# Kernel optimization log

Hardware: AMD Instinct MI355X
Metric: run time of the kernel (lower is better)

Reference implementation:

```python
import jax, jax.numpy as jnp
import numpy as np

EPS = 1e-6


def setup_inputs() -> dict:
    key = jax.random.key(0)
    k1, k2, k3 = jax.random.split(key, 3)
    B, L, H, D = 4, 4096, 16, 64
    return {
        "queries": jax.random.normal(k1, (B, L, H, D), dtype=jnp.float32),
        "keys": jax.random.normal(k2, (B, L, H, D), dtype=jnp.float32),
        "values": jax.random.normal(k3, (B, L, H, D), dtype=jnp.float32),
        "attn_mask": jnp.zeros((1,), dtype=bool),  # unused, matches torch signature
    }


def reference(queries, keys, values, attn_mask):
    # [B, L, H, D] -> [B, H, L, D]
    q = jax.nn.sigmoid(jnp.transpose(queries, (0, 2, 1, 3)))
    k = jax.nn.sigmoid(jnp.transpose(keys, (0, 2, 1, 3)))
    v = jnp.transpose(values, (0, 2, 1, 3))
    L = q.shape[2]
    S = k.shape[2]

    # flow normalizers (incoming / outgoing)
    normalizer_row = 1.0 / jnp.einsum('nhld,nhd->nhl', q + EPS, k.sum(axis=2) + EPS)
    normalizer_col = 1.0 / jnp.einsum('nhsd,nhd->nhs', k + EPS, q.sum(axis=2) + EPS)

    # competitive refinement
    row_refine = jnp.einsum(
        'nhld,nhd->nhl', q + EPS, (k * normalizer_col[..., None]).sum(axis=2) + EPS)
    col_refine = jnp.einsum(
        'nhsd,nhd->nhs', k + EPS, (q * normalizer_row[..., None]).sum(axis=2) + EPS)
    row_refine = jax.nn.sigmoid(row_refine * (float(L) / float(S)))
    col_refine = jax.nn.softmax(col_refine, axis=-1) * S

    # kv: [B, H, D, D]
    kv = jnp.einsum('nhsd,nhse->nhde', k, v * col_refine[..., None])
    x = jnp.einsum('nhld,nhde->nhle', q, kv)
    x = x * normalizer_row[..., None] * row_refine[..., None]
    # back to [B, L, H, D]
    return jnp.transpose(x, (0, 2, 1, 3))
```

## Files before the change

kernel.cpp:

```cpp
#include <hip/hip_runtime.h>
#include <math.h>
#include <stdint.h>

#define B_ 4
#define L_ 4096
#define H_ 16
#define EPSF 1e-6f
#define STR 66
#define STRO 68

typedef short bf16x8 __attribute__((ext_vector_type(8)));
typedef float f32x4 __attribute__((ext_vector_type(4)));
union FragU { uint32_t u[4]; bf16x8 v; };

__device__ __forceinline__ float sigf(float x) { return 1.0f / (1.0f + __expf(-x)); }

__device__ __forceinline__ uint32_t packhl(float x) {
    uint32_t xb = __float_as_uint(x);
    uint32_t hb = xb & 0xFFFF0000u;
    float lo = x - __uint_as_float(hb);
    return (hb >> 16) | (__float_as_uint(lo) & 0xFFFF0000u);
}

__device__ __forceinline__ void buildfrag(const uint32_t w[8], bf16x8& hi, bf16x8& lo) {
    FragU H, L;
#pragma unroll
    for (int t = 0; t < 4; ++t) {
        H.u[t] = __builtin_amdgcn_perm(w[2 * t + 1], w[2 * t], 0x05040100u);
        L.u[t] = __builtin_amdgcn_perm(w[2 * t + 1], w[2 * t], 0x07060302u);
    }
    hi = H.v; lo = L.v;
}

#define MFMA3(acc, ahi, alo, bhi, blo)                                        \
    acc = __builtin_amdgcn_mfma_f32_16x16x32_bf16(ahi, bhi, acc, 0, 0, 0);    \
    acc = __builtin_amdgcn_mfma_f32_16x16x32_bf16(ahi, blo, acc, 0, 0, 0);    \
    acc = __builtin_amdgcn_mfma_f32_16x16x32_bf16(alo, bhi, acc, 0, 0, 0);

__global__ __launch_bounds__(256, 8) void k_ksum(const float* __restrict__ K,
                                                 float* __restrict__ ksum) {
    int bh = blockIdx.x, b = bh >> 4, h = bh & 15;
    int t = threadIdx.x, lane = t & 63, w = t >> 6;
    int q4 = lane >> 4, i16 = lane & 15;
    int r0 = blockIdx.y * 128 + w * 32;
    float a0 = 0.f, a1 = 0.f, a2 = 0.f, a3 = 0.f;
#pragma unroll
    for (int ib = 0; ib < 2; ++ib) {
        float4 x[4];
#pragma unroll
        for (int j = 0; j < 4; ++j) {
            int r = r0 + (ib * 4 + j) * 4 + q4;
            x[j] = *(const float4*)(K + (((size_t)b * L_ + r) * H_ + h) * 64 + 4 * i16);
        }
#pragma unroll
        for (int j = 0; j < 4; ++j) {
            a0 += sigf(x[j].x); a1 += sigf(x[j].y);
            a2 += sigf(x[j].z); a3 += sigf(x[j].w);
        }
    }
#pragma unroll
    for (int m = 16; m < 64; m <<= 1) {
        a0 += __shfl_xor(a0, m, 64); a1 += __shfl_xor(a1, m, 64);
        a2 += __shfl_xor(a2, m, 64); a3 += __shfl_xor(a3, m, 64);
    }
    if (q4 == 0) {
        atomicAdd(&ksum[bh * 64 + 4 * i16 + 0], a0);
        atomicAdd(&ksum[bh * 64 + 4 * i16 + 1], a1);
        atomicAdd(&ksum[bh * 64 + 4 * i16 + 2], a2);
        atomicAdd(&ksum[bh * 64 + 4 * i16 + 3], a3);
    }
}

__global__ __launch_bounds__(256, 6) void k_qpass(const float* __restrict__ Q,
                                                  const float* __restrict__ ksum,
                                                  float* __restrict__ qsum,
                                                  float* __restrict__ qn) {
    int bh = blockIdx.x, b = bh >> 4, h = bh & 15;
    int t = threadIdx.x, lane = t & 63, w = t >> 6;
    int q4 = lane >> 4, i16 = lane & 15;
    int r0 = blockIdx.y * 128 + w * 32;
    float4 ks4 = *(const float4*)(ksum + bh * 64 + 4 * i16);
    ks4.x += EPSF; ks4.y += EPSF; ks4.z += EPSF; ks4.w += EPSF;
    float qs0 = 0.f, qs1 = 0.f, qs2 = 0.f, qs3 = 0.f;
    float qa0 = 0.f, qa1 = 0.f, qa2 = 0.f, qa3 = 0.f;
#pragma unroll
    for (int ib = 0; ib < 2; ++ib) {
        float4 x[4];
#pragma unroll
        for (int j = 0; j < 4; ++j) {
            int r = r0 + (ib * 4 + j) * 4 + q4;
            x[j] = *(const float4*)(Q + (((size_t)b * L_ + r) * H_ + h) * 64 + 4 * i16);
        }
#pragma unroll
        for (int j = 0; j < 4; ++j) {
            float s0 = sigf(x[j].x), s1 = sigf(x[j].y), s2 = sigf(x[j].z), s3 = sigf(x[j].w);
            float pa = (s0 + EPSF) * ks4.x + (s1 + EPSF) * ks4.y +
                       (s2 + EPSF) * ks4.z + (s3 + EPSF) * ks4.w;
#pragma unroll
            for (int m = 1; m < 16; m <<= 1) pa += __shfl_xor(pa, m, 64);
            float nr = __builtin_amdgcn_rcpf(pa);
            qs0 += s0; qs1 += s1; qs2 += s2; qs3 += s3;
            qa0 += s0 * nr; qa1 += s1 * nr; qa2 += s2 * nr; qa3 += s3 * nr;
        }
    }
#pragma unroll
    for (int m = 16; m < 64; m <<= 1) {
        qs0 += __shfl_xor(qs0, m, 64); qs1 += __shfl_xor(qs1, m, 64);
        qs2 += __shfl_xor(qs2, m, 64); qs3 += __shfl_xor(qs3, m, 64);
        qa0 += __shfl_xor(qa0, m, 64); qa1 += __shfl_xor(qa1, m, 64);
        qa2 += __shfl_xor(qa2, m, 64); qa3 += __shfl_xor(qa3, m, 64);
    }
    if (q4 == 0) {
        atomicAdd(&qsum[bh * 64 + 4 * i16 + 0], qs0);
        atomicAdd(&qsum[bh * 64 + 4 * i16 + 1], qs1);
        atomicAdd(&qsum[bh * 64 + 4 * i16 + 2], qs2);
        atomicAdd(&qsum[bh * 64 + 4 * i16 + 3], qs3);
        atomicAdd(&qn[bh * 64 + 4 * i16 + 0], qa0);
        atomicAdd(&qn[bh * 64 + 4 * i16 + 1], qa1);
        atomicAdd(&qn[bh * 64 + 4 * i16 + 2], qa2);
        atomicAdd(&qn[bh * 64 + 4 * i16 + 3], qa3);
    }
}

__global__ __launch_bounds__(256, 4) void k_kv(const float* __restrict__ K,
                                               const float* __restrict__ V,
                                               const float* __restrict__ qsum,
                                               const float* __restrict__ qn,
                                               float* __restrict__ kn,
                                               float* __restrict__ den,
                                               float* __restrict__ KVp) {
    int bh = blockIdx.x, b = bh >> 4, h = bh & 15;
    int t = threadIdx.x, lane = t & 63, w = t >> 6;
    int q4 = lane >> 4, i16 = lane & 15;
    __shared__ uint32_t skp[64 * STR];
    __shared__ uint32_t vwp[64 * STR];
    float4 qsE = *(const float4*)(qsum + bh * 64 + 4 * i16);
    float4 qnE = *(const float4*)(qn + bh * 64 + 4 * i16);
    qsE.x += EPSF; qsE.y += EPSF; qsE.z += EPSF; qsE.w += EPSF;
    qnE.x += EPSF; qnE.y += EPSF; qnE.z += EPSF; qnE.w += EPSF;
    f32x4 acc[4];
#pragma unroll
    for (int tm = 0; tm < 4; ++tm) acc[tm] = (f32x4){0.f, 0.f, 0.f, 0.f};
    float kn0 = 0.f, kn1 = 0.f, kn2 = 0.f, kn3 = 0.f, dacc = 0.f;
    int rowbase = blockIdx.y * 256;
    float4 kx[4], vx[4];
#pragma unroll
    for (int j = 0; j < 4; ++j) {
        int r = rowbase + w * 16 + j * 4 + q4;
        size_t off = (((size_t)b * L_ + r) * H_ + h) * 64 + 4 * i16;
        kx[j] = *(const float4*)(K + off);
        vx[j] = *(const float4*)(V + off);
    }
#pragma unroll
    for (int tile = 0; tile < 4; ++tile) {
#pragma unroll
        for (int j = 0; j < 4; ++j) {
            int lr = w * 16 + j * 4 + q4;
            float s0 = sigf(kx[j].x), s1 = sigf(kx[j].y), s2 = sigf(kx[j].z), s3 = sigf(kx[j].w);
            float pa = (s0 + EPSF) * qsE.x + (s1 + EPSF) * qsE.y +
                       (s2 + EPSF) * qsE.z + (s3 + EPSF) * qsE.w;
            float pc = (s0 + EPSF) * qnE.x + (s1 + EPSF) * qnE.y +
                       (s2 + EPSF) * qnE.z + (s3 + EPSF) * qnE.w;
#pragma unroll
            for (int m = 1; m < 16; m <<= 1) {
                pa += __shfl_xor(pa, m, 64);
                pc += __shfl_xor(pc, m, 64);
            }
            float ncol = __builtin_amdgcn_rcpf(pa);
            float es = __expf(pc);
            kn0 += s0 * ncol; kn1 += s1 * ncol; kn2 += s2 * ncol; kn3 += s3 * ncol;
            if (i16 == 0) dacc += es;
            uint32_t* sp = &skp[lr * STR + 4 * i16];
            *(uint2*)sp = make_uint2(packhl(s0), packhl(s1));
            *(uint2*)(sp + 2) = make_uint2(packhl(s2), packhl(s3));
            uint32_t* vp = &vwp[lr * STR + 4 * i16];
            *(uint2*)vp = make_uint2(packhl(vx[j].x * es), packhl(vx[j].y * es));
            *(uint2*)(vp + 2) = make_uint2(packhl(vx[j].z * es), packhl(vx[j].w * es));
        }
        float4 kx2[4], vx2[4];
        if (tile < 3) {
#pragma unroll
            for (int j = 0; j < 4; ++j) {
                int r = rowbase + (tile + 1) * 64 + w * 16 + j * 4 + q4;
                size_t off = (((size_t)b * L_ + r) * H_ + h) * 64 + 4 * i16;
                kx2[j] = *(const float4*)(K + off);
                vx2[j] = *(const float4*)(V + off);
            }
        }
        __syncthreads();
#pragma unroll
        for (int ks = 0; ks < 2; ++ks) {
            uint32_t bw[8];
#pragma unroll
            for (int j = 0; j < 8; ++j)
                bw[j] = vwp[(32 * ks + 8 * q4 + j) * STR + 16 * w + i16];
            bf16x8 bhi, blo; buildfrag(bw, bhi, blo);
#pragma unroll
            for (int tm = 0; tm < 4; ++tm) {
                uint32_t aw[8];
#pragma unroll
                for (int j = 0; j < 8; ++j)
                    aw[j] = skp[(32 * ks + 8 * q4 + j) * STR + 16 * tm + i16];
                bf16x8 ahi, alo; buildfrag(aw, ahi, alo);
                MFMA3(acc[tm], ahi, alo, bhi, blo);
            }
        }
        __syncthreads();
        if (tile < 3) {
#pragma unroll
            for (int j = 0; j < 4; ++j) { kx[j] = kx2[j]; vx[j] = vx2[j]; }
        }
    }
    float* kvslice = KVp + ((size_t)blockIdx.y * 64 + bh) * 4096;
#pragma unroll
    for (int tm = 0; tm < 4; ++tm)
#pragma unroll
        for (int r = 0; r < 4; ++r)
            kvslice[(16 * tm + 4 * q4 + r) * 64 + 16 * w + i16] = acc[tm][r];
#pragma unroll
    for (int m = 16; m < 64; m <<= 1) {
        kn0 += __shfl_xor(kn0, m, 64); kn1 += __shfl_xor(kn1, m, 64);
        kn2 += __shfl_xor(kn2, m, 64); kn3 += __shfl_xor(kn3, m, 64);
    }
    if (q4 == 0) {
        atomicAdd(&kn[bh * 64 + 4 * i16 + 0], kn0);
        atomicAdd(&kn[bh * 64 + 4 * i16 + 1], kn1);
        atomicAdd(&kn[bh * 64 + 4 * i16 + 2], kn2);
        atomicAdd(&kn[bh * 64 + 4 * i16 + 3], kn3);
    }
#pragma unroll
    for (int m = 1; m < 64; m <<= 1) dacc += __shfl_xor(dacc, m, 64);
    if (lane == 0) atomicAdd(&den[bh], dacc);
}

__global__ __launch_bounds__(256) void k_reduce(const float* __restrict__ KVp,
                                                float* __restrict__ KVg) {
    int bh = blockIdx.x;
    int f4 = blockIdx.y * 256 + threadIdx.x;
    float4 acc = make_float4(0.f, 0.f, 0.f, 0.f);
#pragma unroll
    for (int p = 0; p < 16; ++p) {
        float4 x = *(const float4*)(KVp + ((size_t)p * 64 + bh) * 4096 + 4 * f4);
        acc.x += x.x; acc.y += x.y; acc.z += x.z; acc.w += x.w;
    }
    *(float4*)(KVg + (size_t)bh * 4096 + 4 * f4) = acc;
}

__global__ __launch_bounds__(256, 4) void k_out(const float* __restrict__ Q,
                                                const float* __restrict__ ksum,
                                                const float* __restrict__ kn,
                                                const float* __restrict__ den,
                                                const float* __restrict__ KVg,
                                                float* __restrict__ out) {
    int bh = blockIdx.x, b = bh >> 4, h = bh & 15;
    int t = threadIdx.x, lane = t & 63, w = t >> 6;
    int q4 = lane >> 4, i16 = lane & 15;
    __shared__ uint32_t kvt[64 * STRO];
    __shared__ uint32_t sqp[4][16 * STRO];
    __shared__ float scale_s[4][16];
    float4 ksE = *(const float4*)(ksum + bh * 64 + 4 * i16);
    float4 knE = *(const float4*)(kn + bh * 64 + 4 * i16);
    ksE.x += EPSF; ksE.y += EPSF; ksE.z += EPSF; ksE.w += EPSF;
    knE.x += EPSF; knE.y += EPSF; knE.z += EPSF; knE.w += EPSF;
    float sden = 4096.0f * __builtin_amdgcn_rcpf(den[bh]);
#pragma unroll
    for (int i = 0; i < 4; ++i) {
        int f4 = t + i * 256;
        float4 x = *(const float4*)(KVg + (size_t)bh * 4096 + 4 * f4);
        int d = (4 * f4) & 63, e = f4 >> 4;
        kvt[(d + 0) * STRO + e] = packhl(x.x);
        kvt[(d + 1) * STRO + e] = packhl(x.y);
        kvt[(d + 2) * STRO + e] = packhl(x.z);
        kvt[(d + 3) * STRO + e] = packhl(x.w);
    }
    int rowbase = blockIdx.y * 256;
    float4 qx[4];
#pragma unroll
    for (int j = 0; j < 4; ++j) {
        int r = rowbase + w * 64 + j * 4 + q4;
        qx[j] = *(const float4*)(Q + (((size_t)b * L_ + r) * H_ + h) * 64 + 4 * i16);
    }
    __syncthreads();
#pragma unroll
    for (int g = 0; g < 4; ++g) {
        int r0 = rowbase + w * 64 + g * 16;
#pragma unroll
        for (int j = 0; j < 4; ++j) {
            int lr = j * 4 + q4;
            float s0 = sigf(qx[j].x), s1 = sigf(qx[j].y), s2 = sigf(qx[j].z), s3 = sigf(qx[j].w);
            float pa = (s0 + EPSF) * ksE.x + (s1 + EPSF) * ksE.y +
                       (s2 + EPSF) * ksE.z + (s3 + EPSF) * ksE.w;
            float pb = (s0 + EPSF) * knE.x + (s1 + EPSF) * knE.y +
                       (s2 + EPSF) * knE.z + (s3 + EPSF) * knE.w;
#pragma unroll
            for (int m = 1; m < 16; m <<= 1) {
                pa += __shfl_xor(pa, m, 64);
                pb += __shfl_xor(pb, m, 64);
            }
            float sc = __builtin_amdgcn_rcpf(pa) * sigf(pb) * sden;
            if (i16 == 0) scale_s[w][lr] = sc;
            uint32_t* sp = &sqp[w][lr * STRO + 4 * i16];
            *(uint4*)sp = make_uint4(packhl(s0), packhl(s1), packhl(s2), packhl(s3));
        }
        float4 qx2[4];
        if (g < 3) {
#pragma unroll
            for (int j = 0; j < 4; ++j) {
                int r = rowbase + w * 64 + (g + 1) * 16 + j * 4 + q4;
                qx2[j] = *(const float4*)(Q + (((size_t)b * L_ + r) * H_ + h) * 64 + 4 * i16);
            }
        }
        f32x4 acc[4];
#pragma unroll
        for (int tn = 0; tn < 4; ++tn) acc[tn] = (f32x4){0.f, 0.f, 0.f, 0.f};
#pragma unroll
        for (int ks = 0; ks < 2; ++ks) {
            const uint32_t* ap = &sqp[w][i16 * STRO + 32 * ks + 8 * q4];
            uint4 a0 = *(const uint4*)ap, a1 = *(const uint4*)(ap + 4);
            uint32_t aw[8] = {a0.x, a0.y, a0.z, a0.w, a1.x, a1.y, a1.z, a1.w};
            bf16x8 ahi, alo; buildfrag(aw, ahi, alo);
#pragma unroll
            for (int tn = 0; tn < 4; ++tn) {
                const uint32_t* bp = &kvt[(16 * tn + i16) * STRO + 32 * ks + 8 * q4];
                uint4 b0 = *(const uint4*)bp, b1 = *(const uint4*)(bp + 4);
                uint32_t bw[8] = {b0.x, b0.y, b0.z, b0.w, b1.x, b1.y, b1.z, b1.w};
                bf16x8 bhi, blo; buildfrag(bw, bhi, blo);
                MFMA3(acc[tn], ahi, alo, bhi, blo);
            }
        }
#pragma unroll
        for (int tn = 0; tn < 4; ++tn)
#pragma unroll
            for (int r = 0; r < 4; ++r) {
                int rl = 4 * q4 + r;
                float sc = scale_s[w][rl];
                out[(((size_t)b * L_ + (r0 + rl)) * H_ + h) * 64 + 16 * tn + i16] =
                    acc[tn][r] * sc;
            }
        if (g < 3) {
#pragma unroll
            for (int j = 0; j < 4; ++j) qx[j] = qx2[j];
        }
    }
}

extern "C" void kernel_launch(void* const* d_in, const int* in_sizes, int n_in,
                              void* d_out, int out_size, void* d_ws, size_t ws_size,
                              hipStream_t stream) {
    const float* Q = (const float*)d_in[0];
    const float* K = (const float*)d_in[1];
    const float* V = (const float*)d_in[2];
    float* out = (float*)d_out;
    float* ws = (float*)d_ws;
    float* ksum = ws;
    float* qsum = ws + 4096;
    float* qn   = ws + 8192;
    float* kn   = ws + 12288;
    float* den  = ws + 16384;
    float* KVg  = ws + 16448;
    float* KVp  = ws + 16448 + 262144;

    hipMemsetAsync(d_ws, 0, 16448ull * 4ull, stream);
    k_ksum<<<dim3(64, 32), 256, 0, stream>>>(K, ksum);
    k_qpass<<<dim3(64, 32), 256, 0, stream>>>(Q, ksum, qsum, qn);
    k_kv<<<dim3(64, 16), 256, 0, stream>>>(K, V, qsum, qn, kn, den, KVp);
    k_reduce<<<dim3(64, 4), 256, 0, stream>>>(KVp, KVg);
    k_out<<<dim3(64, 16), 256, 0, stream>>>(Q, ksum, kn, den, KVg, out);
}
```

Baseline: 308.2 us.

## Use DPP row reductions, deeper load prefetch, and 2x2 MFMA tiling in kv kernel

Replaces the 16-lane shfl_xor reductions with DPP row operations, which avoids the LDS-routed shuffle traffic. The ksum and qpass kernels now issue all eight row loads up front for more memory-level parallelism, and ksum's launch-bounds occupancy hint is lowered to 6. The kv kernel double-buffers K/V register tiles two tiles ahead and gives each wave a 2x2 block of MFMA output tiles, so it reuses B fragments instead of rebuilding four A fragments per wave. The cost is higher register pressure, which could reduce occupancy.

```diff
diff --git a/kernel.cpp b/kernel.cpp
--- a/kernel.cpp
+++ b/kernel.cpp
@@ -15,6 +15,14 @@
 
 __device__ __forceinline__ float sigf(float x) { return 1.0f / (1.0f + __expf(-x)); }
 
+__device__ __forceinline__ float rowsum16(float v) {
+    v += __int_as_float(__builtin_amdgcn_update_dpp(0, __float_as_int(v), 0xB1, 0xF, 0xF, true));
+    v += __int_as_float(__builtin_amdgcn_update_dpp(0, __float_as_int(v), 0x4E, 0xF, 0xF, true));
+    v += __int_as_float(__builtin_amdgcn_update_dpp(0, __float_as_int(v), 0x124, 0xF, 0xF, true));
+    v += __int_as_float(__builtin_amdgcn_update_dpp(0, __float_as_int(v), 0x128, 0xF, 0xF, true));
+    return v;
+}
+
 __device__ __forceinline__ uint32_t packhl(float x) {
     uint32_t xb = __float_as_uint(x);
     uint32_t hb = xb & 0xFFFF0000u;
@@ -37,26 +45,23 @@
     acc = __builtin_amdgcn_mfma_f32_16x16x32_bf16(ahi, blo, acc, 0, 0, 0);    \
     acc = __builtin_amdgcn_mfma_f32_16x16x32_bf16(alo, bhi, acc, 0, 0, 0);
 
-__global__ __launch_bounds__(256, 8) void k_ksum(const float* __restrict__ K,
+__global__ __launch_bounds__(256, 6) void k_ksum(const float* __restrict__ K,
                                                  float* __restrict__ ksum) {
     int bh = blockIdx.x, b = bh >> 4, h = bh & 15;
     int t = threadIdx.x, lane = t & 63, w = t >> 6;
     int q4 = lane >> 4, i16 = lane & 15;
     int r0 = blockIdx.y * 128 + w * 32;
+    float4 x[8];
+#pragma unroll
+    for (int j = 0; j < 8; ++j) {
+        int r = r0 + j * 4 + q4;
+        x[j] = *(const float4*)(K + (((size_t)b * L_ + r) * H_ + h) * 64 + 4 * i16);
+    }
     float a0 = 0.f, a1 = 0.f, a2 = 0.f, a3 = 0.f;
 #pragma unroll
-    for (int ib = 0; ib < 2; ++ib) {
-        float4 x[4];
-#pragma unroll
-        for (int j = 0; j < 4; ++j) {
-            int r = r0 + (ib * 4 + j) * 4 + q4;
-            x[j] = *(const float4*)(K + (((size_t)b * L_ + r) * H_ + h) * 64 + 4 * i16);
-        }
-#pragma unroll
-        for (int j = 0; j < 4; ++j) {
-            a0 += sigf(x[j].x); a1 += sigf(x[j].y);
-            a2 += sigf(x[j].z); a3 += sigf(x[j].w);
-        }
+    for (int j = 0; j < 8; ++j) {
+        a0 += sigf(x[j].x); a1 += sigf(x[j].y);
+        a2 += sigf(x[j].z); a3 += sigf(x[j].w);
     }
 #pragma unroll
     for (int m = 16; m < 64; m <<= 1) {
@@ -81,27 +86,23 @@
     int r0 = blockIdx.y * 128 + w * 32;
     float4 ks4 = *(const float4*)(ksum + bh * 64 + 4 * i16);
     ks4.x += EPSF; ks4.y += EPSF; ks4.z += EPSF; ks4.w += EPSF;
+    float4 x[8];
+#pragma unroll
+    for (int j = 0; j < 8; ++j) {
+        int r = r0 + j * 4 + q4;
+        x[j] = *(const float4*)(Q + (((size_t)b * L_ + r) * H_ + h) * 64 + 4 * i16);
+    }
     float qs0 = 0.f, qs1 = 0.f, qs2 = 0.f, qs3 = 0.f;
     float qa0 = 0.f, qa1 = 0.f, qa2 = 0.f, qa3 = 0.f;
 #pragma unroll
-    for (int ib = 0; ib < 2; ++ib) {
-        float4 x[4];
-#pragma unroll
-        for (int j = 0; j < 4; ++j) {
-            int r = r0 + (ib * 4 + j) * 4 + q4;
-            x[j] = *(const float4*)(Q + (((size_t)b * L_ + r) * H_ + h) * 64 + 4 * i16);
-        }
-#pragma unroll
-        for (int j = 0; j < 4; ++j) {
-            float s0 = sigf(x[j].x), s1 = sigf(x[j].y), s2 = sigf(x[j].z), s3 = sigf(x[j].w);
-            float pa = (s0 + EPSF) * ks4.x + (s1 + EPSF) * ks4.y +
-                       (s2 + EPSF) * ks4.z + (s3 + EPSF) * ks4.w;
-#pragma unroll
-            for (int m = 1; m < 16; m <<= 1) pa += __shfl_xor(pa, m, 64);
-            float nr = __builtin_amdgcn_rcpf(pa);
-            qs0 += s0; qs1 += s1; qs2 += s2; qs3 += s3;
-            qa0 += s0 * nr; qa1 += s1 * nr; qa2 += s2 * nr; qa3 += s3 * nr;
-        }
+    for (int j = 0; j < 8; ++j) {
+        float s0 = sigf(x[j].x), s1 = sigf(x[j].y), s2 = sigf(x[j].z), s3 = sigf(x[j].w);
+        float pa = (s0 + EPSF) * ks4.x + (s1 + EPSF) * ks4.y +
+                   (s2 + EPSF) * ks4.z + (s3 + EPSF) * ks4.w;
+        pa = rowsum16(pa);
+        float nr = __builtin_amdgcn_rcpf(pa);
+        qs0 += s0; qs1 += s1; qs2 += s2; qs3 += s3;
+        qa0 += s0 * nr; qa1 += s1 * nr; qa2 += s2 * nr; qa3 += s3 * nr;
     }
 #pragma unroll
     for (int m = 16; m < 64; m <<= 1) {
@@ -119,6 +120,73 @@
         atomicAdd(&qn[bh * 64 + 4 * i16 + 1], qa1);
         atomicAdd(&qn[bh * 64 + 4 * i16 + 2], qa2);
         atomicAdd(&qn[bh * 64 + 4 * i16 + 3], qa3);
+    }
+}
+
+__device__ __forceinline__ void kv_load(const float* Kp, const float* Vp,
+                                        int rowbase, int tile, int lrow,
+                                        float4* kx, float4* vx) {
+#pragma unroll
+    for (int j = 0; j < 4; ++j) {
+        size_t r = (size_t)(rowbase + tile * 64 + lrow + j * 4) * 1024;
+        kx[j] = *(const float4*)(Kp + r);
+        vx[j] = *(const float4*)(Vp + r);
+    }
+}
+
+__device__ __forceinline__ void kv_stage(const float4* kx, const float4* vx,
+                                         int w, int q4, int i16,
+                                         float4 qsE, float4 qnE,
+                                         uint32_t* skp, uint32_t* vwp,
+                                         float& kn0, float& kn1, float& kn2, float& kn3,
+                                         float& dacc) {
+#pragma unroll
+    for (int j = 0; j < 4; ++j) {
+        int lr = w * 16 + j * 4 + q4;
+        float s0 = sigf(kx[j].x), s1 = sigf(kx[j].y), s2 = sigf(kx[j].z), s3 = sigf(kx[j].w);
+        float pa = (s0 + EPSF) * qsE.x + (s1 + EPSF) * qsE.y +
+                   (s2 + EPSF) * qsE.z + (s3 + EPSF) * qsE.w;
+        float pc = (s0 + EPSF) * qnE.x + (s1 + EPSF) * qnE.y +
+                   (s2 + EPSF) * qnE.z + (s3 + EPSF) * qnE.w;
+        pa = rowsum16(pa); pc = rowsum16(pc);
+        float ncol = __builtin_amdgcn_rcpf(pa);
+        float es = __expf(pc);
+        kn0 += s0 * ncol; kn1 += s1 * ncol; kn2 += s2 * ncol; kn3 += s3 * ncol;
+        if (i16 == 0) dacc += es;
+        uint32_t* sp = &skp[lr * STR + 4 * i16];
+        *(uint2*)sp = make_uint2(packhl(s0), packhl(s1));
+        *(uint2*)(sp + 2) = make_uint2(packhl(s2), packhl(s3));
+        uint32_t* vp = &vwp[lr * STR + 4 * i16];
+        *(uint2*)vp = make_uint2(packhl(vx[j].x * es), packhl(vx[j].y * es));
+        *(uint2*)(vp + 2) = make_uint2(packhl(vx[j].z * es), packhl(vx[j].w * es));
+    }
+}
+
+__device__ __forceinline__ void kv_mfma(const uint32_t* skp, const uint32_t* vwp,
+                                        int q4, int i16, int td0, int te0, f32x4* acc) {
+#pragma unroll
+    for (int ks = 0; ks < 2; ++ks) {
+        bf16x8 bhi[2], blo[2];
+#pragma unroll
+        for (int tn = 0; tn < 2; ++tn) {
+            uint32_t bw[8];
+#pragma unroll
+            for (int j = 0; j < 8; ++j)
+                bw[j] = vwp[(32 * ks + 8 * q4 + j) * STR + 16 * (te0 + tn) + i16];
+            buildfrag(bw, bhi[tn], blo[tn]);
+        }
+#pragma unroll
+        for (int tm = 0; tm < 2; ++tm) {
+            uint32_t aw[8];
+#pragma unroll
+            for (int j = 0; j < 8; ++j)
+                aw[j] = skp[(32 * ks + 8 * q4 + j) * STR + 16 * (td0 + tm) + i16];
+            bf16x8 ahi, alo; buildfrag(aw, ahi, alo);
+#pragma unroll
+            for (int tn = 0; tn < 2; ++tn) {
+                MFMA3(acc[tm * 2 + tn], ahi, alo, bhi[tn], blo[tn]);
+            }
+        }
     }
 }
 
@@ -132,6 +200,7 @@
     int bh = blockIdx.x, b = bh >> 4, h = bh & 15;
     int t = threadIdx.x, lane = t & 63, w = t >> 6;
     int q4 = lane >> 4, i16 = lane & 15;
+    int td0 = (w >> 1) * 2, te0 = (w & 1) * 2;
     __shared__ uint32_t skp[64 * STR];
     __shared__ uint32_t vwp[64 * STR];
     float4 qsE = *(const float4*)(qsum + bh * 64 + 4 * i16);
@@ -143,80 +212,41 @@
     for (int tm = 0; tm < 4; ++tm) acc[tm] = (f32x4){0.f, 0.f, 0.f, 0.f};
     float kn0 = 0.f, kn1 = 0.f, kn2 = 0.f, kn3 = 0.f, dacc = 0.f;
     int rowbase = blockIdx.y * 256;
-    float4 kx[4], vx[4];
-#pragma unroll
-    for (int j = 0; j < 4; ++j) {
-        int r = rowbase + w * 16 + j * 4 + q4;
-        size_t off = (((size_t)b * L_ + r) * H_ + h) * 64 + 4 * i16;
-        kx[j] = *(const float4*)(K + off);
-        vx[j] = *(const float4*)(V + off);
-    }
-#pragma unroll
-    for (int tile = 0; tile < 4; ++tile) {
-#pragma unroll
-        for (int j = 0; j < 4; ++j) {
-            int lr = w * 16 + j * 4 + q4;
-            float s0 = sigf(kx[j].x), s1 = sigf(kx[j].y), s2 = sigf(kx[j].z), s3 = sigf(kx[j].w);
-            float pa = (s0 + EPSF) * qsE.x + (s1 + EPSF) * qsE.y +
-                       (s2 + EPSF) * qsE.z + (s3 + EPSF) * qsE.w;
-            float pc = (s0 + EPSF) * qnE.x + (s1 + EPSF) * qnE.y +
-                       (s2 + EPSF) * qnE.z + (s3 + EPSF) * qnE.w;
-#pragma unroll
-            for (int m = 1; m < 16; m <<= 1) {
-                pa += __shfl_xor(pa, m, 64);
-                pc += __shfl_xor(pc, m, 64);
-            }
-            float ncol = __builtin_amdgcn_rcpf(pa);
-            float es = __expf(pc);
-            kn0 += s0 * ncol; kn1 += s1 * ncol; kn2 += s2 * ncol; kn3 += s3 * ncol;
-            if (i16 == 0) dacc += es;
-            uint32_t* sp = &skp[lr * STR + 4 * i16];
-            *(uint2*)sp = make_uint2(packhl(s0), packhl(s1));
-            *(uint2*)(sp + 2) = make_uint2(packhl(s2), packhl(s3));
-            uint32_t* vp = &vwp[lr * STR + 4 * i16];
-            *(uint2*)vp = make_uint2(packhl(vx[j].x * es), packhl(vx[j].y * es));
-            *(uint2*)(vp + 2) = make_uint2(packhl(vx[j].z * es), packhl(vx[j].w * es));
-        }
-        float4 kx2[4], vx2[4];
-        if (tile < 3) {
-#pragma unroll
-            for (int j = 0; j < 4; ++j) {
-                int r = rowbase + (tile + 1) * 64 + w * 16 + j * 4 + q4;
-                size_t off = (((size_t)b * L_ + r) * H_ + h) * 64 + 4 * i16;
-                kx2[j] = *(const float4*)(K + off);
-                vx2[j] = *(const float4*)(V + off);
-            }
-        }
-        __syncthreads();
-#pragma unroll
-        for (int ks = 0; ks < 2; ++ks) {
-            uint32_t bw[8];
-#pragma unroll
-            for (int j = 0; j < 8; ++j)
-                bw[j] = vwp[(32 * ks + 8 * q4 + j) * STR + 16 * w + i16];
-            bf16x8 bhi, blo; buildfrag(bw, bhi, blo);
-#pragma unroll
-            for (int tm = 0; tm < 4; ++tm) {
-                uint32_t aw[8];
-#pragma unroll
-                for (int j = 0; j < 8; ++j)
-                    aw[j] = skp[(32 * ks + 8 * q4 + j) * STR + 16 * tm + i16];
-                bf16x8 ahi, alo; buildfrag(aw, ahi, alo);
-                MFMA3(acc[tm], ahi, alo, bhi, blo);
-            }
-        }
-        __syncthreads();
-        if (tile < 3) {
-#pragma unroll
-            for (int j = 0; j < 4; ++j) { kx[j] = kx2[j]; vx[j] = vx2[j]; }
-        }
-    }
+    size_t base = (((size_t)b * L_) * H_ + h) * 64 + 4 * i16;
+    const float* Kp = K + base;
+    const float* Vp = V + base;
+    int lrow = w * 16 + q4;
+
+    float4 kA[4], vA[4], kB[4], vB[4];
+    kv_load(Kp, Vp, rowbase, 0, lrow, kA, vA);
+    kv_load(Kp, Vp, rowbase, 1, lrow, kB, vB);
+    kv_stage(kA, vA, w, q4, i16, qsE, qnE, skp, vwp, kn0, kn1, kn2, kn3, dacc);
+    __syncthreads();
+    kv_mfma(skp, vwp, q4, i16, td0, te0, acc);
+    __syncthreads();
+    kv_load(Kp, Vp, rowbase, 2, lrow, kA, vA);
+    kv_stage(kB, vB, w, q4, i16, qsE, qnE, skp, vwp, kn0, kn1, kn2, kn3, dacc);
+    __syncthreads();
+    kv_mfma(skp, vwp, q4, i16, td0, te0, acc);
+    __syncthreads();
+    kv_load(Kp, Vp, rowbase, 3, lrow, kB, vB);
+    kv_stage(kA, vA, w, q4, i16, qsE, qnE, skp, vwp, kn0, kn1, kn2, kn3, dacc);
+    __syncthreads();
+    kv_mfma(skp, vwp, q4, i16, td0, te0, acc);
+    __syncthreads();
+    kv_stage(kB, vB, w, q4, i16, qsE, qnE, skp, vwp, kn0, kn1, kn2, kn3, dacc);
+    __syncthreads();
+    kv_mfma(skp, vwp, q4, i16, td0, te0, acc);
+
     float* kvslice = KVp + ((size_t)blockIdx.y * 64 + bh) * 4096;
 #pragma unroll
-    for (int tm = 0; tm < 4; ++tm)
-#pragma unroll
-        for (int r = 0; r < 4; ++r)
-            kvslice[(16 * tm + 4 * q4 + r) * 64 + 16 * w + i16] = acc[tm][r];
+    for (int tm = 0; tm < 2; ++tm)
+#pragma unroll
+        for (int tn = 0; tn < 2; ++tn)
+#pragma unroll
+            for (int r = 0; r < 4; ++r)
+                kvslice[(16 * (td0 + tm) + 4 * q4 + r) * 64 + 16 * (te0 + tn) + i16] =
+                    acc[tm * 2 + tn][r];
 #pragma unroll
     for (int m = 16; m < 64; m <<= 1) {
         kn0 += __shfl_xor(kn0, m, 64); kn1 += __shfl_xor(kn1, m, 64);
@@ -244,6 +274,25 @@
         acc.x += x.x; acc.y += x.y; acc.z += x.z; acc.w += x.w;
     }
     *(float4*)(KVg + (size_t)bh * 4096 + 4 * f4) = acc;
+}
+
+__device__ __forceinline__ void out_stage(const float4* qx, int w, int q4, int i16,
+                                          float4 ksE, float4 knE, float sden,
+                                          uint32_t* sqpw, float* scalew) {
+#pragma unroll
+    for (int j = 0; j < 4; ++j) {
+        int lr = j * 4 + q4;
+        float s0 = sigf(qx[j].x), s1 = sigf(qx[j].y), s2 = sigf(qx[j].z), s3 = sigf(qx[j].w);
+        float pa = (s0 + EPSF) * ksE.x + (s1 + EPSF) * ksE.y +
+                   (s2 + EPSF) * ksE.z + (s3 + EPSF) * ksE.w;
+        float pb = (s0 + EPSF) * knE.x + (s1 + EPSF) * knE.y +
+                   (s2 + EPSF) * knE.z + (s3 + EPSF) * knE.w;
+        pa = rowsum16(pa); pb = rowsum16(pb);
+        float sc = __builtin_amdgcn_rcpf(pa) * sigf(pb) * sden;
+        if (i16 == 0) scalew[lr] = sc;
+        uint32_t* sp = &sqpw[lr * STRO + 4 * i16];
+        *(uint4*)sp = make_uint4(packhl(s0), packhl(s1), packhl(s2), packhl(s3));
+    }
 }
 
 __global__ __launch_bounds__(256, 4) void k_out(const float* __restrict__ Q,
@@ -263,51 +312,36 @@
     ksE.x += EPSF; ksE.y += EPSF; ksE.z += EPSF; ksE.w += EPSF;
     knE.x += EPSF; knE.y += EPSF; knE.z += EPSF; knE.w += EPSF;
     float sden = 4096.0f * __builtin_amdgcn_rcpf(den[bh]);
+    int rowbase = blockIdx.y * 256;
+    size_t base = (((size_t)b * L_) * H_ + h) * 64 + 4 * i16;
+    const float* Qp = Q + base;
+    float4 qx[4];
+#pragma unroll
+    for (int j = 0; j < 4; ++j) {
+        size_t r = (size_t)(rowbase + w * 64 + j * 4 + q4) * 1024;
+        qx[j] = *(const float4*)(Qp + r);
+    }
 #pragma unroll
     for (int i = 0; i < 4; ++i) {
-        int f4 = t + i * 256;
-        float4 x = *(const float4*)(KVg + (size_t)bh * 4096 + 4 * f4);
-        int d = (4 * f4) & 63, e = f4 >> 4;
+        int f4i = t + i * 256;
+        float4 x = *(const float4*)(KVg + (size_t)bh * 4096 + 4 * f4i);
+        int d = (4 * f4i) & 63, e = f4i >> 4;
         kvt[(d + 0) * STRO + e] = packhl(x.x);
         kvt[(d + 1) * STRO + e] = packhl(x.y);
         kvt[(d + 2) * STRO + e] = packhl(x.z);
         kvt[(d + 3) * STRO + e] = packhl(x.w);
     }
-    int rowbase = blockIdx.y * 256;
-    float4 qx[4];
-#pragma unroll
-    for (int j = 0; j < 4; ++j) {
-        int r = rowbase + w * 64 + j * 4 + q4;
-        qx[j] = *(const float4*)(Q + (((size_t)b * L_ + r) * H_ + h) * 64 + 4 * i16);
-    }
     __syncthreads();
 #pragma unroll
     for (int g = 0; g < 4; ++g) {
         int r0 = rowbase + w * 64 + g * 16;
-#pragma unroll
-        for (int j = 0; j < 4; ++j) {
-            int lr = j * 4 + q4;
-            float s0 = sigf(qx[j].x), s1 = sigf(qx[j].y), s2 = sigf(qx[j].z), s3 = sigf(qx[j].w);
-            float pa = (s0 + EPSF) * ksE.x + (s1 + EPSF) * ksE.y +
-                       (s2 + EPSF) * ksE.z + (s3 + EPSF) * ksE.w;
-            float pb = (s0 + EPSF) * knE.x + (s1 + EPSF) * knE.y +
-                       (s2 + EPSF) * knE.z + (s3 + EPSF) * knE.w;
-#pragma unroll
-            for (int m = 1; m < 16; m <<= 1) {
-                pa += __shfl_xor(pa, m, 64);
-                pb += __shfl_xor(pb, m, 64);
-            }
-            float sc = __builtin_amdgcn_rcpf(pa) * sigf(pb) * sden;
-            if (i16 == 0) scale_s[w][lr] = sc;
-            uint32_t* sp = &sqp[w][lr * STRO + 4 * i16];
-            *(uint4*)sp = make_uint4(packhl(s0), packhl(s1), packhl(s2), packhl(s3));
-        }
+        out_stage(qx, w, q4, i16, ksE, knE, sden, &sqp[w][0], &scale_s[w][0]);
         float4 qx2[4];
         if (g < 3) {
 #pragma unroll
             for (int j = 0; j < 4; ++j) {
-                int r = rowbase + w * 64 + (g + 1) * 16 + j * 4 + q4;
-                qx2[j] = *(const float4*)(Q + (((size_t)b * L_ + r) * H_ + h) * 64 + 4 * i16);
+                size_t r = (size_t)(rowbase + w * 64 + (g + 1) * 16 + j * 4 + q4) * 1024;
+                qx2[j] = *(const float4*)(Qp + r);
             }
         }
         f32x4 acc[4];
```

After: 342.8 us. 1.11x slower.
